# Performance work log

Hardware: AMD Instinct MI355X
Metric: run time of the kernel (lower is better)

## Reference

```python
import jax, jax.numpy as jnp
import numpy as np

NUM_CHANNELS = 64
IN_FEATURES = 256
OUT_FEATURES = 256
B = 128
N = 2048


def setup_inputs() -> dict:
    key = jax.random.key(0)
    k_x, k_c, k_w, k_b = jax.random.split(key, 4)
    x = jax.random.normal(k_x, (B, N, IN_FEATURES), dtype=jnp.float32)
    channels = jax.random.randint(k_c, (N,), 0, NUM_CHANNELS, dtype=jnp.int64)
    # kaiming_uniform_(a=sqrt(5)) over fan_in -> bound = 1/sqrt(fan_in)
    wb = 1.0 / np.sqrt(IN_FEATURES)
    weight = jax.random.uniform(k_w, (NUM_CHANNELS, OUT_FEATURES, IN_FEATURES),
                                dtype=jnp.float32, minval=-wb, maxval=wb)
    bias = jax.random.uniform(k_b, (NUM_CHANNELS, OUT_FEATURES),
                              dtype=jnp.float32, minval=-wb, maxval=wb)
    return {"x": x, "channels": channels, "weight": weight, "bias": bias}


def reference(x, channels, weight, bias):
    # Gather per-point weights/biases by channel id (shared across batch).
    w = weight[channels]          # [N, out, in]
    b = bias[channels]            # [N, out]
    # Equivalent to bmm over the point axis: [B,N,in] x [N,out,in] -> [B,N,out]
    y = jnp.einsum('bni,noi->bno', x, w)
    y = y + b                     # broadcast over batch
    y = jnp.tanh(y)               # activation=True
    y = y + x                     # residual mode 1 (out == in)
    return (y, channels)
```

## Files before the change

kernel.cpp:

```cpp
#include <hip/hip_runtime.h>
#include <hip/hip_bf16.h>


#define B_SZ  128
#define N_SZ  2048
#define IN_F  256
#define OUT_F 256

typedef __attribute__((ext_vector_type(8))) __bf16 bf16x8;
typedef __attribute__((ext_vector_type(4))) float  f32x4;

__device__ __forceinline__ unsigned f2bf1(float f) {
    union { float f; unsigned u; } v; v.f = f;
    return (v.u + 0x7fffu + ((v.u >> 16) & 1u)) >> 16;
}
__device__ __forceinline__ int pack2(float lo, float hi) {
    return (int)(f2bf1(lo) | (f2bf1(hi) << 16));
}
__device__ __forceinline__ float bf2f(unsigned short u) {
    union { unsigned u; float f; } v; v.u = ((unsigned)u) << 16;
    return v.f;
}
__device__ __forceinline__ float tanh_fast(float s) {
    float a = fabsf(s);
    float t = __expf(-2.0f * a);
    float r = (1.0f - t) * __builtin_amdgcn_rcpf(1.0f + t);
    return s < 0.0f ? -r : r;
}

__global__ __launch_bounds__(512, 4) void channel_dense_kernel(
    const float* __restrict__ x, const int* __restrict__ channels,
    const float* __restrict__ weight, const float* __restrict__ bias,
    float* __restrict__ y)
{
    __shared__ __align__(16) unsigned char smem[65536 + 16384];
    unsigned char* sA = smem;
    unsigned char* sB = smem + 65536;

    const int n   = blockIdx.x;
    const int tid = threadIdx.x;
    const int c   = channels[n];
    const float* wch = weight + (size_t)c * (OUT_F * IN_F);

    {
        const int row = tid >> 2;
        const int sub = tid & 3;
        const float* xrow = x + ((size_t)row * N_SZ + n) * IN_F + sub * 64;
        const int swz = (row & 15) << 4;
        #pragma unroll
        for (int j = 0; j < 8; ++j) {
            float4 f0 = *(const float4*)(xrow + j * 8);
            float4 f1 = *(const float4*)(xrow + j * 8 + 4);
            int4 p;
            p.x = pack2(f0.x, f0.y); p.y = pack2(f0.z, f0.w);
            p.z = pack2(f1.x, f1.y); p.w = pack2(f1.z, f1.w);
            int byte = (row * 512 + (sub * 64 + j * 8) * 2) ^ swz;
            *(int4*)(sA + byte) = p;
        }
    }

    const int bo = tid >> 1;
    const int bh = tid & 1;
    const int bswz = (bo & 3) << 4;
    auto stageB = [&](int kt) {
        const float* wrow = wch + (size_t)bo * IN_F + kt * 32 + bh * 16;
        float4 f0 = *(const float4*)(wrow);
        float4 f1 = *(const float4*)(wrow + 4);
        float4 f2 = *(const float4*)(wrow + 8);
        float4 f3 = *(const float4*)(wrow + 12);
        int4 p0, p1;
        p0.x = pack2(f0.x, f0.y); p0.y = pack2(f0.z, f0.w);
        p0.z = pack2(f1.x, f1.y); p0.w = pack2(f1.z, f1.w);
        p1.x = pack2(f2.x, f2.y); p1.y = pack2(f2.z, f2.w);
        p1.z = pack2(f3.x, f3.y); p1.w = pack2(f3.z, f3.w);
        int base = bo * 64 + bh * 32;
        *(int4*)(sB + ((base)      ^ bswz)) = p0;
        *(int4*)(sB + ((base + 16) ^ bswz)) = p1;
    };
    stageB(0);
    __syncthreads();

    const int wv   = tid >> 6;
    const int lane = tid & 63;
    const int wr   = wv >> 2;
    const int wc   = wv & 3;
    const int lr   = lane & 15;
    const int lkb  = (lane >> 4) * 16;

    f32x4 acc[4][4] = {};

    for (int kt = 0; kt < 8; ++kt) {
        bf16x8 af[4], bfr[4];
        #pragma unroll
        for (int m = 0; m < 4; ++m) {
            int row  = wr * 64 + m * 16 + lr;
            int byte = (row * 512 + kt * 64 + lkb) ^ ((row & 15) << 4);
            af[m] = *(const bf16x8*)(sA + byte);
        }
        #pragma unroll
        for (int nf = 0; nf < 4; ++nf) {
            int o    = wc * 64 + nf * 16 + lr;
            int byte = (o * 64 + lkb) ^ ((o & 3) << 4);
            bfr[nf] = *(const bf16x8*)(sB + byte);
        }
        #pragma unroll
        for (int m = 0; m < 4; ++m)
            #pragma unroll
            for (int nf = 0; nf < 4; ++nf)
                acc[m][nf] = __builtin_amdgcn_mfma_f32_16x16x32_bf16(af[m], bfr[nf], acc[m][nf], 0, 0, 0);

        if (kt < 7) {
            __syncthreads();
            stageB(kt + 1);
            __syncthreads();
        }
    }

    const float* bch = bias + (size_t)c * OUT_F;
    #pragma unroll
    for (int m = 0; m < 4; ++m) {
        #pragma unroll
        for (int r = 0; r < 4; ++r) {
            int brow = wr * 64 + m * 16 + (lane >> 4) * 4 + r;
            float* yrow = y + ((size_t)brow * N_SZ + n) * OUT_F;
            int aswz = (brow & 15) << 4;
            #pragma unroll
            for (int nf = 0; nf < 4; ++nf) {
                int o = wc * 64 + nf * 16 + lr;
                float s = acc[m][nf][r] + bch[o];
                float t = tanh_fast(s);
                unsigned short us = *(const unsigned short*)(sA + ((brow * 512 + o * 2) ^ aswz));
                yrow[o] = t + bf2f(us);
            }
        }
    }
}

__global__ void channels_copy_kernel(const int* __restrict__ ch, float* __restrict__ out) {
    int i = blockIdx.x * 256 + threadIdx.x;
    if (i < N_SZ) out[i] = (float)ch[i];
}

extern "C" void kernel_launch(void* const* d_in, const int* in_sizes, int n_in,
                              void* d_out, int out_size, void* d_ws, size_t ws_size,
                              hipStream_t stream) {
    const float* x        = (const float*)d_in[0];
    const int*   channels = (const int*)d_in[1];
    const float* weight   = (const float*)d_in[2];
    const float* bias     = (const float*)d_in[3];
    float* y = (float*)d_out;

    channel_dense_kernel<<<dim3(N_SZ), dim3(512), 0, stream>>>(x, channels, weight, bias, y);
    channels_copy_kernel<<<dim3(N_SZ / 256), dim3(256), 0, stream>>>(
        channels, y + (size_t)B_SZ * N_SZ * OUT_F);
}
```

Before: 202.6 us.

## Swap MFMA operand roles, retile x in LDS, prefetch weights, vectorize stores

Swaps the MFMA operands so weights form the A side and x the B side. Each lane's accumulator then holds four consecutive output features, so the epilogue can write float4 stores and read the residual as packed bf16 pairs. x in LDS is reorganised into per-k-tile 8KB slabs with a new swizzle, and the weight tile for step kt+2 is loaded into registers while kt+1 is written to LDS, which hides global latency. The change trades more live registers and a fully unrolled k-loop for coalesced output writes and fewer LDS reads.

```diff
diff --git a/kernel.cpp b/kernel.cpp
--- a/kernel.cpp
+++ b/kernel.cpp
@@ -4,8 +4,6 @@
 
 #define B_SZ  128
 #define N_SZ  2048
-#define IN_F  256
-#define OUT_F 256
 
 typedef __attribute__((ext_vector_type(8))) __bf16 bf16x8;
 typedef __attribute__((ext_vector_type(4))) float  f32x4;
@@ -17,8 +15,8 @@
 __device__ __forceinline__ int pack2(float lo, float hi) {
     return (int)(f2bf1(lo) | (f2bf1(hi) << 16));
 }
-__device__ __forceinline__ float bf2f(unsigned short u) {
-    union { unsigned u; float f; } v; v.u = ((unsigned)u) << 16;
+__device__ __forceinline__ float bf2f(unsigned u16) {
+    union { unsigned u; float f; } v; v.u = u16 << 16;
     return v.f;
 }
 __device__ __forceinline__ float tanh_fast(float s) {
@@ -40,13 +38,36 @@
     const int n   = blockIdx.x;
     const int tid = threadIdx.x;
     const int c   = channels[n];
-    const float* wch = weight + (size_t)c * (OUT_F * IN_F);
+    const float* wch = weight + (size_t)c * 65536;
+
+    const int bo = tid >> 1;
+    const int bh = tid & 1;
+    const float* wbase = wch + bo * 256 + bh * 16;
+    float4 w0, w1, w2, w3;
+    #define WLOAD(kt) do { const float* p_ = wbase + (kt) * 32;             \
+        w0 = *(const float4*)(p_);     w1 = *(const float4*)(p_ + 4);       \
+        w2 = *(const float4*)(p_ + 8); w3 = *(const float4*)(p_ + 12); } while (0)
+
+    const int sb_lin   = bo * 64 + bh * 32;
+    const int sb_swz   = (bo & 7) << 4;
+    const int sb_byte0 = (sb_lin)      ^ sb_swz;
+    const int sb_byte1 = (sb_lin + 16) ^ sb_swz;
+    #define SB_WRITE() do {                                                 \
+        int4 q0, q1;                                                        \
+        q0.x = pack2(w0.x, w0.y); q0.y = pack2(w0.z, w0.w);                 \
+        q0.z = pack2(w1.x, w1.y); q0.w = pack2(w1.z, w1.w);                 \
+        q1.x = pack2(w2.x, w2.y); q1.y = pack2(w2.z, w2.w);                 \
+        q1.z = pack2(w3.x, w3.y); q1.w = pack2(w3.z, w3.w);                 \
+        *(int4*)(sB + sb_byte0) = q0;                                       \
+        *(int4*)(sB + sb_byte1) = q1; } while (0)
+
+    WLOAD(0);
 
     {
         const int row = tid >> 2;
         const int sub = tid & 3;
-        const float* xrow = x + ((size_t)row * N_SZ + n) * IN_F + sub * 64;
-        const int swz = (row & 15) << 4;
+        const float* xrow = x + ((size_t)row * N_SZ + n) * 256 + sub * 64;
+        const int swz = (row & 7) << 4;
         #pragma unroll
         for (int j = 0; j < 8; ++j) {
             float4 f0 = *(const float4*)(xrow + j * 8);
@@ -54,86 +75,72 @@
             int4 p;
             p.x = pack2(f0.x, f0.y); p.y = pack2(f0.z, f0.w);
             p.z = pack2(f1.x, f1.y); p.w = pack2(f1.z, f1.w);
-            int byte = (row * 512 + (sub * 64 + j * 8) * 2) ^ swz;
+            int byte = (sub * 2 + (j >> 2)) * 8192 + ((row * 64 + (j & 3) * 16) ^ swz);
             *(int4*)(sA + byte) = p;
         }
     }
 
-    const int bo = tid >> 1;
-    const int bh = tid & 1;
-    const int bswz = (bo & 3) << 4;
-    auto stageB = [&](int kt) {
-        const float* wrow = wch + (size_t)bo * IN_F + kt * 32 + bh * 16;
-        float4 f0 = *(const float4*)(wrow);
-        float4 f1 = *(const float4*)(wrow + 4);
-        float4 f2 = *(const float4*)(wrow + 8);
-        float4 f3 = *(const float4*)(wrow + 12);
-        int4 p0, p1;
-        p0.x = pack2(f0.x, f0.y); p0.y = pack2(f0.z, f0.w);
-        p0.z = pack2(f1.x, f1.y); p0.w = pack2(f1.z, f1.w);
-        p1.x = pack2(f2.x, f2.y); p1.y = pack2(f2.z, f2.w);
-        p1.z = pack2(f3.x, f3.y); p1.w = pack2(f3.z, f3.w);
-        int base = bo * 64 + bh * 32;
-        *(int4*)(sB + ((base)      ^ bswz)) = p0;
-        *(int4*)(sB + ((base + 16) ^ bswz)) = p1;
-    };
-    stageB(0);
+    SB_WRITE();
+    WLOAD(1);
     __syncthreads();
 
+    const int lane = tid & 63;
     const int wv   = tid >> 6;
-    const int lane = tid & 63;
-    const int wr   = wv >> 2;
-    const int wc   = wv & 3;
+    const int wo   = wv & 3;
+    const int wb   = wv >> 2;
     const int lr   = lane & 15;
-    const int lkb  = (lane >> 4) * 16;
+    const int lg4  = lane >> 4;
+    const int lane_part = ((lr * 64 + lg4 * 16) ^ ((lr & 7) << 4));
+    const int wf_base = lane_part + wo * 4096;
+    const int xf_base = lane_part + wb * 4096;
 
     f32x4 acc[4][4] = {};
 
+    #pragma unroll
     for (int kt = 0; kt < 8; ++kt) {
-        bf16x8 af[4], bfr[4];
+        bf16x8 wf[4], xf[4];
         #pragma unroll
-        for (int m = 0; m < 4; ++m) {
-            int row  = wr * 64 + m * 16 + lr;
-            int byte = (row * 512 + kt * 64 + lkb) ^ ((row & 15) << 4);
-            af[m] = *(const bf16x8*)(sA + byte);
-        }
+        for (int mo = 0; mo < 4; ++mo)
+            wf[mo] = *(const bf16x8*)(sB + wf_base + mo * 1024);
         #pragma unroll
-        for (int nf = 0; nf < 4; ++nf) {
-            int o    = wc * 64 + nf * 16 + lr;
-            int byte = (o * 64 + lkb) ^ ((o & 3) << 4);
-            bfr[nf] = *(const bf16x8*)(sB + byte);
-        }
+        for (int nb = 0; nb < 4; ++nb)
+            xf[nb] = *(const bf16x8*)(sA + xf_base + nb * 1024 + kt * 8192);
         #pragma unroll
-        for (int m = 0; m < 4; ++m)
+        for (int mo = 0; mo < 4; ++mo)
             #pragma unroll
-            for (int nf = 0; nf < 4; ++nf)
-                acc[m][nf] = __builtin_amdgcn_mfma_f32_16x16x32_bf16(af[m], bfr[nf], acc[m][nf], 0, 0, 0);
+            for (int nb = 0; nb < 4; ++nb)
+                acc[mo][nb] = __builtin_amdgcn_mfma_f32_16x16x32_bf16(wf[mo], xf[nb], acc[mo][nb], 0, 0, 0);
 
         if (kt < 7) {
             __syncthreads();
-            stageB(kt + 1);
+            SB_WRITE();
+            if (kt < 6) WLOAD(kt + 2);
             __syncthreads();
         }
     }
 
-    const float* bch = bias + (size_t)c * OUT_F;
+    const float* bch = bias + (size_t)c * 256;
     #pragma unroll
-    for (int m = 0; m < 4; ++m) {
+    for (int mo = 0; mo < 4; ++mo) {
+        const int o0 = wo * 64 + mo * 16 + lg4 * 4;
+        const float4 bv = *(const float4*)(bch + o0);
+        const int kt_r  = o0 >> 5;
+        const int intra = (o0 & 31) * 2;
         #pragma unroll
-        for (int r = 0; r < 4; ++r) {
-            int brow = wr * 64 + m * 16 + (lane >> 4) * 4 + r;
-            float* yrow = y + ((size_t)brow * N_SZ + n) * OUT_F;
-            int aswz = (brow & 15) << 4;
-            #pragma unroll
-            for (int nf = 0; nf < 4; ++nf) {
-                int o = wc * 64 + nf * 16 + lr;
-                float s = acc[m][nf][r] + bch[o];
-                float t = tanh_fast(s);
-                unsigned short us = *(const unsigned short*)(sA + ((brow * 512 + o * 2) ^ aswz));
-                yrow[o] = t + bf2f(us);
-            }
+        for (int nb = 0; nb < 4; ++nb) {
+            const int b = wb * 64 + nb * 16 + lr;
+            const int rbyte = kt_r * 8192 + ((b * 64 + intra) ^ ((b & 7) << 4));
+            uint2 rv = *(const uint2*)(sA + rbyte);
+            float4 out;
+            out.x = tanh_fast(acc[mo][nb][0] + bv.x) + bf2f(rv.x & 0xffffu);
+            out.y = tanh_fast(acc[mo][nb][1] + bv.y) + bf2f(rv.x >> 16);
+            out.z = tanh_fast(acc[mo][nb][2] + bv.z) + bf2f(rv.y & 0xffffu);
+            out.w = tanh_fast(acc[mo][nb][3] + bv.w) + bf2f(rv.y >> 16);
+            *(float4*)(y + ((size_t)b * N_SZ + n) * 256 + o0) = out;
         }
     }
+    #undef WLOAD
+    #undef SB_WRITE
 }
 
 __global__ void channels_copy_kernel(const int* __restrict__ ch, float* __restrict__ out) {
@@ -152,5 +159,5 @@
 
     channel_dense_kernel<<<dim3(N_SZ), dim3(512), 0, stream>>>(x, channels, weight, bias, y);
     channels_copy_kernel<<<dim3(N_SZ / 256), dim3(256), 0, stream>>>(
-        channels, y + (size_t)B_SZ * N_SZ * OUT_F);
+        channels, y + (size_t)B_SZ * N_SZ * 256);
 }
```

After: 219.4 us. 8.3% more time.
